# Performance work log

Hardware: AMD Instinct MI355X
Metric: run time of the kernel (lower is better)

Reference implementation:

```python
import jax, jax.numpy as jnp
import numpy as np

# module hyperparams (init_kwargs)
IN_SIZE = 64      # D
OUT_SIZE = 64     # D_
NUM_CLUSTER = 8   # K
HEADS = 4         # H
GAMMA = 1.0
TAU = 10.0

E = 400000        # num edges
N_NODES = 50000


def setup_inputs() -> dict:
    key = jax.random.key(0)
    ks = jax.random.split(key, 8)
    msg = jax.random.normal(ks[0], (E, OUT_SIZE), dtype=jnp.float32)
    x_i = jax.random.normal(ks[1], (E, IN_SIZE), dtype=jnp.float32)
    x_j = jax.random.normal(ks[2], (E, IN_SIZE), dtype=jnp.float32)
    e_ij = jax.random.normal(ks[3], (E, IN_SIZE), dtype=jnp.float32)
    index = jax.random.randint(ks[4], (E,), 0, N_NODES, dtype=jnp.int32)
    # xavier-uniform-ish cluster centers [H, K, D]
    lim = float(np.sqrt(6.0 / (NUM_CLUSTER + IN_SIZE)))
    k = jax.random.uniform(ks[5], (HEADS, NUM_CLUSTER, IN_SIZE), dtype=jnp.float32,
                           minval=-lim, maxval=lim)
    # final Linear(K*D_ -> D_), stored as [in, out]
    limw = float(np.sqrt(1.0 / (NUM_CLUSTER * OUT_SIZE)))
    W = jax.random.uniform(ks[6], (NUM_CLUSTER * OUT_SIZE, OUT_SIZE), dtype=jnp.float32,
                           minval=-limw, maxval=limw)
    b = jax.random.uniform(ks[7], (OUT_SIZE,), dtype=jnp.float32, minval=-limw, maxval=limw)
    return {"msg": msg, "x_i": x_i, "x_j": x_j, "e_ij": e_ij, "index": index,
            "num_nodes": N_NODES, "k": k, "W": W, "b": b}


def reference(msg, x_i, x_j, e_ij, index, num_nodes, k, W, b):
    H, K, D, D_ = HEADS, NUM_CLUSTER, IN_SIZE, OUT_SIZE
    # agg_q = elementwise sum of neighbor features and edge features -> [E, D]
    x = x_j + e_ij
    kf = k.reshape(H * K, D)
    # squared euclidean distances: [H*K, E]
    dist = (jnp.sum(kf * kf, axis=1)[:, None]
            + jnp.sum(x * x, axis=1)[None, :]
            - 2.0 * (kf @ x.T))
    dist = jnp.maximum(dist, 0.0)
    # Student-t kernel
    t = (1.0 + dist / GAMMA) ** (-(GAMMA + 1.0) / 2.0)
    t = t.reshape(H, K, -1).transpose(2, 1, 0)  # [E, K, H]
    w = t / jnp.sum(t, axis=1, keepdims=True) * TAU  # normalize over clusters
    w = jax.nn.softmax(jnp.mean(w, axis=-1), axis=-1)  # [E, K]
    # weight messages per cluster -> [E, K*D_]
    new_msg = (w[:, :, None] * msg[:, None, :]).reshape(-1, K * D_)
    agg = jax.ops.segment_sum(new_msg, index, num_segments=num_nodes)  # [N, K*D_]
    out = agg @ W + b
    return jax.nn.leaky_relu(out, negative_slope=0.01)
```

## Files before the change

### kernel.cpp

```cpp
#include <hip/hip_runtime.h>
#include <hip/hip_bf16.h>

typedef unsigned short u16;
typedef unsigned int   u32;
typedef unsigned long long u64;

typedef __attribute__((ext_vector_type(8))) short  short8;
typedef __attribute__((ext_vector_type(4))) float  floatx4;
typedef __attribute__((ext_vector_type(2))) __fp16 half2v;

#define FIX_SCALE 65536.0f
#define FIX_INV   (1.0f / 65536.0f)
#define FIX_BIAS  (1 << 26)

__device__ __forceinline__ u32 rne_pack(float lo, float hi) {
  u32 bl = __float_as_uint(lo), bh = __float_as_uint(hi);
  u32 rl = ((bl + 0x7FFFu + ((bl >> 16) & 1u)) >> 16) & 0xFFFFu;
  u32 rh = (bh + 0x7FFFu + ((bh >> 16) & 1u)) & 0xFFFF0000u;
  return rl | rh;
}

__device__ __forceinline__ u32 pk_f16(float lo, float hi) {
  half2v h = __builtin_amdgcn_cvt_pkrtz(lo, hi);
  return *(u32*)&h;
}
__device__ __forceinline__ float2 unpk_f16(u32 v) {
  half2v h = *(half2v*)&v;
  return make_float2((float)h.x, (float)h.y);
}

__device__ __forceinline__ short8 scale_frag(uint4 mraw, float w) {
  const u32* in = (const u32*)&mraw;
  uint4 o; u32* ou = (u32*)&o;
  #pragma unroll
  for (int i = 0; i < 4; ++i) {
    float lo = __uint_as_float(in[i] << 16) * w;
    float hi = __uint_as_float(in[i]) * w;
    ou[i] = __builtin_amdgcn_perm(__float_as_uint(hi), __float_as_uint(lo), 0x07060302u);
  }
  return *(short8*)&o;
}

__global__ __launch_bounds__(512, 2) void fused_kernel(
    const float* __restrict__ msg, const float* __restrict__ xj,
    const float* __restrict__ eij, const float* __restrict__ kc,
    const float* __restrict__ Wg, const int* __restrict__ idx,
    u64* __restrict__ o64, int E) {
  __shared__ __align__(16) char un[65536];
  u32*   tl = (u32*)un;
  u16*   Wl = (u16*)un;
  __shared__ __align__(16) u32 wsm[2048];

  const int tid  = threadIdx.x;
  const int lane = tid & 63, wv = tid >> 6;
  const int ln   = lane & 15, q  = lane >> 4;
  const int e0   = blockIdx.x * 512;

  const float4* kc4 = (const float4*)kc;
  short8 af[2][2];
  float knr[2];
  #pragma unroll
  for (int mt = 0; mt < 2; ++mt) {
    float knp = 0.f;
    #pragma unroll
    for (int kk = 0; kk < 2; ++kk) {
      size_t b4 = (size_t)(mt * 16 + ln) * 16 + kk * 8 + q * 2;
      float4 c0 = kc4[b4], c1 = kc4[b4 + 1];
      knp += c0.x*c0.x + c0.y*c0.y + c0.z*c0.z + c0.w*c0.w
           + c1.x*c1.x + c1.y*c1.y + c1.z*c1.z + c1.w*c1.w;
      u32 pk[4] = { rne_pack(c0.x, c0.y), rne_pack(c0.z, c0.w),
                    rne_pack(c1.x, c1.y), rne_pack(c1.z, c1.w) };
      af[mt][kk] = *(short8*)pk;
    }
    knp += __shfl_xor(knp, 16);
    knp += __shfl_xor(knp, 32);
    knr[mt] = knp;
  }
  float kni0[4], kni1[4];
  #pragma unroll
  for (int i = 0; i < 4; ++i) {
    kni0[i] = __shfl(knr[0], q * 4 + i);
    kni1[i] = __shfl(knr[1], q * 4 + i);
  }

  const float4* xj4  = (const float4*)xj;
  const float4* eij4 = (const float4*)eij;
  #pragma unroll
  for (int g = 0; g < 4; ++g) {
    int el = wv * 64 + g * 16 + ln;
    int ge = e0 + el; if (ge >= E) ge = 0;
    size_t b4 = (size_t)ge * 16 + q * 2;
    float4 x0 = xj4[b4],     x1 = xj4[b4 + 1];
    float4 x2 = xj4[b4 + 8], x3 = xj4[b4 + 9];
    float4 ea0 = eij4[b4],     ea1 = eij4[b4 + 1];
    float4 ea2 = eij4[b4 + 8], ea3 = eij4[b4 + 9];
    float s0x = x0.x+ea0.x, s0y = x0.y+ea0.y, s0z = x0.z+ea0.z, s0w = x0.w+ea0.w;
    float s1x = x1.x+ea1.x, s1y = x1.y+ea1.y, s1z = x1.z+ea1.z, s1w = x1.w+ea1.w;
    float s2x = x2.x+ea2.x, s2y = x2.y+ea2.y, s2z = x2.z+ea2.z, s2w = x2.w+ea2.w;
    float s3x = x3.x+ea3.x, s3y = x3.y+ea3.y, s3z = x3.z+ea3.z, s3w = x3.w+ea3.w;
    float ps = s0x*s0x + s0y*s0y + s0z*s0z + s0w*s0w
             + s1x*s1x + s1y*s1y + s1z*s1z + s1w*s1w
             + s2x*s2x + s2y*s2y + s2z*s2z + s2w*s2w
             + s3x*s3x + s3y*s3y + s3z*s3z + s3w*s3w;
    u32 p0[4] = { rne_pack(s0x, s0y), rne_pack(s0z, s0w),
                  rne_pack(s1x, s1y), rne_pack(s1z, s1w) };
    u32 p1[4] = { rne_pack(s2x, s2y), rne_pack(s2z, s2w),
                  rne_pack(s3x, s3y), rne_pack(s3z, s3w) };
    ps += __shfl_xor(ps, 16);
    ps += __shfl_xor(ps, 32);
    short8 bb0 = *(short8*)p0, bb1 = *(short8*)p1;
    floatx4 acc0 = {0.f,0.f,0.f,0.f}, acc1 = {0.f,0.f,0.f,0.f};
    acc0 = __builtin_amdgcn_mfma_f32_16x16x32_bf16(af[0][0], bb0, acc0, 0, 0, 0);
    acc0 = __builtin_amdgcn_mfma_f32_16x16x32_bf16(af[0][1], bb1, acc0, 0, 0, 0);
    acc1 = __builtin_amdgcn_mfma_f32_16x16x32_bf16(af[1][0], bb0, acc1, 0, 0, 0);
    acc1 = __builtin_amdgcn_mfma_f32_16x16x32_bf16(af[1][1], bb1, acc1, 0, 0, 0);
    #pragma unroll
    for (int j = 0; j < 2; ++j) {
      tl[el * 17 + q * 2 + j] =
          pk_f16(kni0[2*j] - 2.f * acc0[2*j], kni0[2*j+1] - 2.f * acc0[2*j+1]);
      tl[el * 17 + 8 + q * 2 + j] =
          pk_f16(kni1[2*j] - 2.f * acc1[2*j], kni1[2*j+1] - 2.f * acc1[2*j+1]);
    }
    if (q == 0) tl[el * 17 + 16] = __float_as_uint(ps);
  }
  __syncthreads();

  {
    int e = tid;
    bool valid = (e0 + e) < E;
    float xn = __uint_as_float(tl[e * 17 + 16]);
    float tv[32];
    float hs[4] = {0.f, 0.f, 0.f, 0.f};
    #pragma unroll
    for (int p = 0; p < 16; ++p) {
      float2 d2 = unpk_f16(tl[e * 17 + p]);
      float dist0 = xn + d2.x; dist0 = dist0 > 0.f ? dist0 : 0.f;
      float dist1 = xn + d2.y; dist1 = dist1 > 0.f ? dist1 : 0.f;
      float t0 = 1.f / (1.f + dist0);
      float t1 = 1.f / (1.f + dist1);
      tv[2*p] = t0; tv[2*p+1] = t1;
      hs[p >> 2] += t0 + t1;
    }
    float r0 = 1.f / hs[0], r1 = 1.f / hs[1], r2 = 1.f / hs[2], r3 = 1.f / hs[3];
    float m[8], mx = -1e30f;
    #pragma unroll
    for (int k = 0; k < 8; ++k) {
      m[k] = 2.5f * (tv[k] * r0 + tv[8 + k] * r1 + tv[16 + k] * r2 + tv[24 + k] * r3);
      mx = m[k] > mx ? m[k] : mx;
    }
    float p[8], sum = 0.f;
    #pragma unroll
    for (int k = 0; k < 8; ++k) { p[k] = __expf(m[k] - mx); sum += p[k]; }
    float rs = valid ? (1.f / sum) : 0.f;
    uint4 wpk = { pk_f16(p[0]*rs, p[1]*rs), pk_f16(p[2]*rs, p[3]*rs),
                  pk_f16(p[4]*rs, p[5]*rs), pk_f16(p[6]*rs, p[7]*rs) };
    *(uint4*)&wsm[e * 4] = wpk;
  }
  __syncthreads();

  #pragma unroll
  for (int it = 0; it < 8; ++it) {
    int c  = (tid >> 6) + it * 8;
    int kk = c >> 2, q2 = c & 3, n = tid & 63;
    const float* src = Wg + (size_t)(kk * 32 + q2 * 8) * 64 + n;
    u32 pk[4];
    #pragma unroll
    for (int jp = 0; jp < 4; ++jp)
      pk[jp] = rne_pack(src[(jp * 2) * 64], src[(jp * 2 + 1) * 64]);
    int tt = (n & 1) + ((n >> 5) << 1);
    int mm = tt * 16 + ((n & 31) >> 1);
    *(uint4*)&Wl[(c * 64 + mm) * 8] = *(uint4*)pk;
  }

  const float4* msg4 = (const float4*)msg;
  uint4 mf[4][2];
  const int edgebase = e0 + wv * 64;
  #pragma unroll
  for (int s = 0; s < 4; ++s) {
    int eg = edgebase + s * 16 + ln; if (eg >= E) eg = E - 1;
    size_t mb = (size_t)eg * 16 + q * 2;
    #pragma unroll
    for (int h = 0; h < 2; ++h) {
      float4 m0 = msg4[mb + h * 8], m1 = msg4[mb + h * 8 + 1];
      u32 pk[4] = { rne_pack(m0.x, m0.y), rne_pack(m0.z, m0.w),
                    rne_pack(m1.x, m1.y), rne_pack(m1.z, m1.w) };
      mf[s][h] = *(uint4*)pk;
    }
  }
  uint4 wf[4];
  #pragma unroll
  for (int s = 0; s < 4; ++s) {
    int eL = wv * 64 + s * 16 + ln;
    wf[s] = *(uint4*)&wsm[eL * 4];
  }
  __syncthreads();

  #pragma unroll
  for (int sp = 0; sp < 2; ++sp) {
    floatx4 acc[2][4];
    #pragma unroll
    for (int u = 0; u < 2; ++u)
      #pragma unroll
      for (int t = 0; t < 4; ++t) { floatx4 z = {0.f,0.f,0.f,0.f}; acc[u][t] = z; }

    #pragma unroll
    for (int kb = 0; kb < 8; ++kb) {
      float w0, w1;
      {
        u32 wd = ((const u32*)&wf[sp * 2])[kb >> 1];
        half2v hv = *(half2v*)&wd;
        w0 = (kb & 1) ? (float)hv.y : (float)hv.x;
      }
      {
        u32 wd = ((const u32*)&wf[sp * 2 + 1])[kb >> 1];
        half2v hv = *(half2v*)&wd;
        w1 = (kb & 1) ? (float)hv.y : (float)hv.x;
      }
      #pragma unroll
      for (int hh = 0; hh < 2; ++hh) {
        int kk = kb * 2 + hh;
        short8 bfr[4];
        #pragma unroll
        for (int t = 0; t < 4; ++t)
          bfr[t] = *(short8*)&Wl[((kk * 4 + q) * 64 + t * 16 + ln) * 8];
        short8 a0 = scale_frag(mf[sp * 2][hh], w0);
        short8 a1 = scale_frag(mf[sp * 2 + 1][hh], w1);
        #pragma unroll
        for (int t = 0; t < 4; ++t) {
          acc[0][t] = __builtin_amdgcn_mfma_f32_16x16x32_bf16(a0, bfr[t], acc[0][t], 0, 0, 0);
          acc[1][t] = __builtin_amdgcn_mfma_f32_16x16x32_bf16(a1, bfr[t], acc[1][t], 0, 0, 0);
        }
      }
    }

    #pragma unroll
    for (int u = 0; u < 2; ++u) {
      int s = sp * 2 + u;
      #pragma unroll
      for (int i = 0; i < 4; ++i) {
        int eg = edgebase + s * 16 + q * 4 + i;
        if (eg < E) {
          int node = idx[eg];
          u64* dst = o64 + (size_t)node * 32 + ln;
          u32 l0 = (u32)((int)rintf(acc[u][0][i] * FIX_SCALE) + FIX_BIAS);
          u32 h0 = (u32)((int)rintf(acc[u][1][i] * FIX_SCALE) + FIX_BIAS);
          u32 l1 = (u32)((int)rintf(acc[u][2][i] * FIX_SCALE) + FIX_BIAS);
          u32 h1 = (u32)((int)rintf(acc[u][3][i] * FIX_SCALE) + FIX_BIAS);
          atomicAdd(dst,      ((u64)h0 << 32) | l0);
          atomicAdd(dst + 16, ((u64)h1 << 32) | l1);
        }
      }
    }
  }
}

__global__ __launch_bounds__(256) void finish_packed(
    u64* __restrict__ a64, const float* __restrict__ b, int ng) {
  int g = blockIdx.x * 256 + threadIdx.x;
  if (g >= ng) return;
  int node = g >> 3, pg = g & 7;
  u64* ap = a64 + (size_t)node * 32 + pg * 4;
  ulonglong4 v = *(ulonglong4*)ap;
  u32 w[8] = { (u32)v.x, (u32)(v.x >> 32), (u32)v.y, (u32)(v.y >> 32),
               (u32)v.z, (u32)(v.z >> 32), (u32)v.w, (u32)(v.w >> 32) };
  u32 cnt = (w[0] + (1u << 25)) >> 26;
  u32 cb  = cnt << 26;
  int col0 = pg * 8;
  float r[8];
  #pragma unroll
  for (int c = 0; c < 8; ++c) {
    float z = (float)(int)(w[c] - cb) * FIX_INV + b[col0 + c];
    r[c] = z > 0.f ? z : 0.01f * z;
  }
  float* op = (float*)a64 + (size_t)node * 64 + col0;
  *(float4*)op       = make_float4(r[0], r[1], r[2], r[3]);
  *(float4*)(op + 4) = make_float4(r[4], r[5], r[6], r[7]);
}

extern "C" void kernel_launch(void* const* d_in, const int* in_sizes, int n_in,
                              void* d_out, int out_size, void* d_ws, size_t ws_size,
                              hipStream_t stream) {
  const float* msg = (const float*)d_in[0];
  const float* xj  = (const float*)d_in[2];
  const float* eij = (const float*)d_in[3];
  const int*   idx = (const int*)d_in[4];
  const float* kc  = (const float*)d_in[6];
  const float* Wg  = (const float*)d_in[7];
  const float* bg  = (const float*)d_in[8];

  int E    = in_sizes[0] / 64;
  int Nout = out_size;
  float* out = (float*)d_out;

  (void)hipMemsetAsync(out, 0, (size_t)Nout * 4, stream);

  int blocks = (E + 511) / 512;
  fused_kernel<<<blocks, 512, 0, stream>>>(msg, xj, eij, kc, Wg, idx,
                                           (u64*)out, E);

  int ng = Nout / 8;
  finish_packed<<<(ng + 255) / 256, 256, 0, stream>>>((u64*)out, bg, ng);
}
```

Before: 422.2 us.

## Sort edges by destination node and merge same-node atomics before scatter

Adds a counting sort of edges by destination index (histogram, single-block scan, scatter) and has the fused kernel process edges in sorted order. Within each lane's four consecutive rows, adjacent edges with the same node are combined in registers before the global 64-bit atomics, which cuts the atomic count and improves locality of output writes. The cost is three extra launches, a serial single-block scan over 50k nodes, and gathered (non-contiguous) reads of msg/x_j/e_ij rows through the permutation. With random indices of about 8 edges per node, few adjacent rows share a node within a group of four.

```diff
diff --git a/kernel.cpp b/kernel.cpp
--- a/kernel.cpp
+++ b/kernel.cpp
@@ -41,20 +41,59 @@
   return *(short8*)&o;
 }
 
+__global__ __launch_bounds__(256) void hist_kernel(
+    const int* __restrict__ idx, u32* __restrict__ hist, int E) {
+  int e = blockIdx.x * 256 + threadIdx.x;
+  if (e < E) atomicAdd(&hist[idx[e]], 1u);
+}
+
+__global__ __launch_bounds__(1024) void scan_kernel(
+    u32* __restrict__ hist, u32* __restrict__ cur, int NN) {
+  __shared__ u32 part[1024];
+  int t = threadIdx.x;
+  int chunk = (NN + 1023) / 1024;
+  int lo = t * chunk, hi = lo + chunk; if (hi > NN) hi = NN; if (lo > NN) lo = NN;
+  u32 s = 0;
+  for (int i = lo; i < hi; ++i) s += hist[i];
+  part[t] = s; __syncthreads();
+  for (int d = 1; d < 1024; d <<= 1) {
+    u32 v = (t >= d) ? part[t - d] : 0; __syncthreads();
+    part[t] += v; __syncthreads();
+  }
+  u32 run = (t > 0) ? part[t - 1] : 0;
+  for (int i = lo; i < hi; ++i) { u32 h = hist[i]; cur[i] = run; run += h; }
+}
+
+__global__ __launch_bounds__(256) void scatter_kernel(
+    const int* __restrict__ idx, u32* __restrict__ cur,
+    u32* __restrict__ order, int E) {
+  int e = blockIdx.x * 256 + threadIdx.x;
+  if (e < E) { u32 p = atomicAdd(&cur[idx[e]], 1u); order[p] = (u32)e; }
+}
+
 __global__ __launch_bounds__(512, 2) void fused_kernel(
     const float* __restrict__ msg, const float* __restrict__ xj,
     const float* __restrict__ eij, const float* __restrict__ kc,
     const float* __restrict__ Wg, const int* __restrict__ idx,
-    u64* __restrict__ o64, int E) {
+    const u32* __restrict__ order, u64* __restrict__ o64, int E) {
   __shared__ __align__(16) char un[65536];
   u32*   tl = (u32*)un;
   u16*   Wl = (u16*)un;
   __shared__ __align__(16) u32 wsm[2048];
+  __shared__ int ordL[512];
+  __shared__ int ndL[512];
 
   const int tid  = threadIdx.x;
   const int lane = tid & 63, wv = tid >> 6;
   const int ln   = lane & 15, q  = lane >> 4;
   const int e0   = blockIdx.x * 512;
+
+  {
+    int oe = 0;
+    if (e0 + tid < E) oe = order ? (int)order[e0 + tid] : (e0 + tid);
+    ordL[tid] = oe;
+    ndL[tid]  = idx[oe];
+  }
 
   const float4* kc4 = (const float4*)kc;
   short8 af[2][2];
@@ -82,13 +121,14 @@
     kni0[i] = __shfl(knr[0], q * 4 + i);
     kni1[i] = __shfl(knr[1], q * 4 + i);
   }
+  __syncthreads();
 
   const float4* xj4  = (const float4*)xj;
   const float4* eij4 = (const float4*)eij;
   #pragma unroll
   for (int g = 0; g < 4; ++g) {
     int el = wv * 64 + g * 16 + ln;
-    int ge = e0 + el; if (ge >= E) ge = 0;
+    int ge = ordL[el];
     size_t b4 = (size_t)ge * 16 + q * 2;
     float4 x0 = xj4[b4],     x1 = xj4[b4 + 1];
     float4 x2 = xj4[b4 + 8], x3 = xj4[b4 + 9];
@@ -174,11 +214,11 @@
 
   const float4* msg4 = (const float4*)msg;
   uint4 mf[4][2];
-  const int edgebase = e0 + wv * 64;
+  const int slotbase = wv * 64;
   #pragma unroll
   for (int s = 0; s < 4; ++s) {
-    int eg = edgebase + s * 16 + ln; if (eg >= E) eg = E - 1;
-    size_t mb = (size_t)eg * 16 + q * 2;
+    int ge = ordL[slotbase + s * 16 + ln];
+    size_t mb = (size_t)ge * 16 + q * 2;
     #pragma unroll
     for (int h = 0; h < 2; ++h) {
       float4 m0 = msg4[mb + h * 8], m1 = msg4[mb + h * 8 + 1];
@@ -190,7 +230,7 @@
   uint4 wf[4];
   #pragma unroll
   for (int s = 0; s < 4; ++s) {
-    int eL = wv * 64 + s * 16 + ln;
+    int eL = slotbase + s * 16 + ln;
     wf[s] = *(uint4*)&wsm[eL * 4];
   }
   __syncthreads();
@@ -236,20 +276,31 @@
     #pragma unroll
     for (int u = 0; u < 2; ++u) {
       int s = sp * 2 + u;
+      int sbase = slotbase + s * 16 + q * 4;
+      u64 P0[4], P1[4]; int N[4]; bool alive[4];
       #pragma unroll
       for (int i = 0; i < 4; ++i) {
-        int eg = edgebase + s * 16 + q * 4 + i;
-        if (eg < E) {
-          int node = idx[eg];
-          u64* dst = o64 + (size_t)node * 32 + ln;
-          u32 l0 = (u32)((int)rintf(acc[u][0][i] * FIX_SCALE) + FIX_BIAS);
-          u32 h0 = (u32)((int)rintf(acc[u][1][i] * FIX_SCALE) + FIX_BIAS);
-          u32 l1 = (u32)((int)rintf(acc[u][2][i] * FIX_SCALE) + FIX_BIAS);
-          u32 h1 = (u32)((int)rintf(acc[u][3][i] * FIX_SCALE) + FIX_BIAS);
-          atomicAdd(dst,      ((u64)h0 << 32) | l0);
-          atomicAdd(dst + 16, ((u64)h1 << 32) | l1);
+        u32 l0 = (u32)((int)rintf(acc[u][0][i] * FIX_SCALE) + FIX_BIAS);
+        u32 h0 = (u32)((int)rintf(acc[u][1][i] * FIX_SCALE) + FIX_BIAS);
+        u32 l1 = (u32)((int)rintf(acc[u][2][i] * FIX_SCALE) + FIX_BIAS);
+        u32 h1 = (u32)((int)rintf(acc[u][3][i] * FIX_SCALE) + FIX_BIAS);
+        P0[i] = ((u64)h0 << 32) | l0;
+        P1[i] = ((u64)h1 << 32) | l1;
+        N[i]  = ndL[sbase + i];
+        alive[i] = (e0 + sbase + i) < E;
+      }
+      #pragma unroll
+      for (int i = 3; i >= 1; --i)
+        if (alive[i] && N[i] == N[i - 1]) {
+          P0[i - 1] += P0[i]; P1[i - 1] += P1[i]; alive[i] = false;
         }
-      }
+      #pragma unroll
+      for (int i = 0; i < 4; ++i)
+        if (alive[i]) {
+          u64* dst = o64 + (size_t)N[i] * 32 + ln;
+          atomicAdd(dst,      P0[i]);
+          atomicAdd(dst + 16, P1[i]);
+        }
     }
   }
 }
@@ -290,12 +341,28 @@
 
   int E    = in_sizes[0] / 64;
   int Nout = out_size;
+  int NN   = Nout / 64;
   float* out = (float*)d_out;
 
+  u32* hist  = (u32*)d_ws;
+  u32* cur   = hist + NN;
+  u32* order = cur + NN;
+  bool use_sort = (d_ws != nullptr) &&
+                  (ws_size >= (size_t)(2 * (size_t)NN + (size_t)E) * 4);
+
   (void)hipMemsetAsync(out, 0, (size_t)Nout * 4, stream);
+
+  if (use_sort) {
+    (void)hipMemsetAsync(hist, 0, (size_t)NN * 4, stream);
+    int eb = (E + 255) / 256;
+    hist_kernel<<<eb, 256, 0, stream>>>(idx, hist, E);
+    scan_kernel<<<1, 1024, 0, stream>>>(hist, cur, NN);
+    scatter_kernel<<<eb, 256, 0, stream>>>(idx, cur, order, E);
+  }
 
   int blocks = (E + 511) / 512;
   fused_kernel<<<blocks, 512, 0, stream>>>(msg, xj, eij, kc, Wg, idx,
+                                           use_sort ? order : (const u32*)nullptr,
                                            (u64*)out, E);
 
   int ng = Nout / 8;
```

Result: slower. 520.6 us (+23.3%).
